# Kernel tuning notes

Hardware: AMD Instinct MI355X
Metric: run time of the kernel (lower is better)

Reference implementation:

```python
import jax, jax.numpy as jnp
import numpy as np

B, T, DM = 4, 1024, 1024
H, NW = 16, 16
HD = DM // H  # 64


def _l2norm(x, eps=1e-12):
    n = jnp.sqrt(jnp.sum(x * x, axis=-1, keepdims=True))
    return x / jnp.maximum(n, eps)


def setup_inputs() -> dict:
    key = jax.random.key(0)
    ks = jax.random.split(key, 14)
    s = 0.02
    d = {
        "x": jax.random.normal(ks[0], (B, T, DM), jnp.float32),
        "Wqf": jax.random.normal(ks[1], (H * NW, DM), jnp.float32) * s,
        "bqf": jnp.zeros((H * NW,), jnp.float32),
        "Wkf": jax.random.normal(ks[2], (H * NW, DM), jnp.float32) * s,
        "bkf": jnp.zeros((H * NW,), jnp.float32),
        "Wqp": jax.random.normal(ks[3], (H * NW, DM), jnp.float32) * s,
        "bqp": jnp.zeros((H * NW,), jnp.float32),
        "Wkp": jax.random.normal(ks[4], (H * NW, DM), jnp.float32) * s,
        "bkp": jnp.zeros((H * NW,), jnp.float32),
        "Wv": jax.random.normal(ks[5], (DM, DM), jnp.float32) * s,
        "bv": jnp.zeros((DM,), jnp.float32),
        "Wo": jax.random.normal(ks[6], (DM, DM), jnp.float32) * s,
        "bo": jnp.zeros((DM,), jnp.float32),
        "inter_scale": jnp.ones((H, 1, 1), jnp.float32),
    }
    return d


def reference(x, Wqf, bqf, Wkf, bkf, Wqp, bqp, Wkp, bkp, Wv, bv, Wo, bo, inter_scale):
    b, t, c = x.shape
    # projections -> [b, H, t, NW]
    def proj(W, bb, w_last):
        return (x @ W.T + bb).reshape(b, t, H, w_last).transpose(0, 2, 1, 3)

    q_f = proj(Wqf, bqf, NW)
    k_f = proj(Wkf, bkf, NW)
    q_p = proj(Wqp, bqp, NW)
    k_p = proj(Wkp, bkp, NW)
    v = proj(Wv, bv, HD)  # [b,H,t,HD]

    t_pos = jnp.arange(t, dtype=x.dtype)[None, None, :, None]  # [1,1,t,1]
    q_waves = jnp.sin(q_f * t_pos + q_p)
    k_waves = jnp.sin(k_f * t_pos + k_p)

    scale_factor = NW ** 0.25
    q_norm = _l2norm(q_waves) * scale_factor
    k_norm = _l2norm(k_waves) * scale_factor

    # wave interference scores [b,H,t,t]
    interference = jnp.einsum('bhtw,bhsw->bhts', q_norm, k_norm)
    interference = interference * inter_scale  # broadcast [H,1,1]

    causal = jnp.tril(jnp.ones((t, t), dtype=bool))  # True = attended
    # elu_plus_one kernel; masked positions -> elu(-inf)+1 == 0
    attn = jnp.where(causal, jax.nn.elu(interference) + 1.0, 0.0)

    num_attended = jnp.arange(1, t + 1, dtype=x.dtype)[None, None, :, None]
    attn = attn / jnp.sqrt(num_attended)

    out = jnp.einsum('bhts,bhsd->bhtd', attn, v)  # [b,H,t,HD]
    out = out.transpose(0, 2, 1, 3).reshape(b, t, c)
    return out @ Wo.T + bo
```

## Files before the change

kernel.cpp:

```cpp
#include <hip/hip_runtime.h>
#include <math.h>

typedef __attribute__((ext_vector_type(8))) short bf16x8;
typedef __attribute__((ext_vector_type(4))) float f32x4;
typedef __attribute__((ext_vector_type(4))) int i32x4;

typedef __attribute__((address_space(3))) void lds_void;
typedef __attribute__((address_space(1))) const void glb_cvoid;

__device__ __forceinline__ unsigned short f32_to_bf16(float f) {
    unsigned u = __float_as_uint(f);
    unsigned r = (u + 0x7FFFu + ((u >> 16) & 1u)) >> 16;
    return (unsigned short)r;
}
__device__ __forceinline__ float bf16_to_f32(unsigned short h) {
    return __uint_as_float(((unsigned)h) << 16);
}

__global__ __launch_bounds__(256)
void split_bf16(const float* __restrict__ src, unsigned short* __restrict__ hi,
                unsigned short* __restrict__ lo, int n4)
{
    const int i = blockIdx.x * 256 + threadIdx.x;
    if (i >= n4) return;
    float4 v = *reinterpret_cast<const float4*>(src + (size_t)i * 4);
    ushort4 h;
    h.x = f32_to_bf16(v.x); h.y = f32_to_bf16(v.y);
    h.z = f32_to_bf16(v.z); h.w = f32_to_bf16(v.w);
    *reinterpret_cast<ushort4*>(hi + (size_t)i * 4) = h;
    if (lo) {
        ushort4 l;
        l.x = f32_to_bf16(v.x - bf16_to_f32(h.x));
        l.y = f32_to_bf16(v.y - bf16_to_f32(h.y));
        l.z = f32_to_bf16(v.z - bf16_to_f32(h.z));
        l.w = f32_to_bf16(v.w - bf16_to_f32(h.w));
        *reinterpret_cast<ushort4*>(lo + (size_t)i * 4) = l;
    }
}

__global__ __launch_bounds__(256)
void split4_bf16(const float* __restrict__ Wqf, const float* __restrict__ Wkf,
                 const float* __restrict__ Wqp, const float* __restrict__ Wkp,
                 unsigned short* __restrict__ WfH, unsigned short* __restrict__ WfL,
                 unsigned short* __restrict__ WpH)
{
    const int i = blockIdx.x * 256 + threadIdx.x;
    const int sel = i >> 16, j = i & 65535;
    const float* W = (sel == 0) ? Wqf : (sel == 1) ? Wkf : (sel == 2) ? Wqp : Wkp;
    float4 v = *reinterpret_cast<const float4*>(W + (size_t)j * 4);
    ushort4 h;
    h.x = f32_to_bf16(v.x); h.y = f32_to_bf16(v.y);
    h.z = f32_to_bf16(v.z); h.w = f32_to_bf16(v.w);
    const size_t o = (size_t)(sel & 1) * 262144 + (size_t)j * 4;
    if (sel < 2) {
        *reinterpret_cast<ushort4*>(WfH + o) = h;
        ushort4 l;
        l.x = f32_to_bf16(v.x - bf16_to_f32(h.x));
        l.y = f32_to_bf16(v.y - bf16_to_f32(h.y));
        l.z = f32_to_bf16(v.z - bf16_to_f32(h.z));
        l.w = f32_to_bf16(v.w - bf16_to_f32(h.w));
        *reinterpret_cast<ushort4*>(WfL + o) = l;
    } else {
        *reinterpret_cast<ushort4*>(WpH + o) = h;
    }
}

__device__ __forceinline__ void xcd_tiles(int& tm, int& tn) {
    const int L = blockIdx.x + gridDim.x * blockIdx.y;
    const int nbn = gridDim.x;
    const int q3 = L >> 3;
    tn = q3 % nbn;
    tm = (L & 7) + 8 * (q3 / nbn);
}

__global__ __launch_bounds__(256)
void freq_gemm_norm(const unsigned short* __restrict__ xh,
                    const unsigned short* __restrict__ xl,
                    const unsigned short* __restrict__ WfH,
                    const unsigned short* __restrict__ WfL,
                    const unsigned short* __restrict__ WpH,
                    const float* __restrict__ bqf, const float* __restrict__ bkf,
                    const float* __restrict__ bqp, const float* __restrict__ bkp,
                    unsigned short* __restrict__ qn, unsigned short* __restrict__ kn)
{
    __shared__ __attribute__((aligned(16))) unsigned short Al[64 * 64];
    __shared__ __attribute__((aligned(16))) unsigned short Bl[64 * 64];

    int tm, tn;
    xcd_tiles(tm, tn);
    const int bm = tm * 64, bn = tn * 64;

    const int tid = threadIdx.x;
    const int w = tid >> 6, l = tid & 63;
    const int wr = w >> 1, wc = w & 1;
    const int lr = l & 15, lg = l >> 4;
    const int r8 = l >> 3;
    const int c8 = l & 7;
    const int csw = (c8 ^ r8) << 3;

    f32x4 accF[2][2], accP[2][2];
#pragma unroll
    for (int i = 0; i < 2; i++)
#pragma unroll
        for (int j = 0; j < 2; j++)
#pragma unroll
            for (int r = 0; r < 4; r++) { accF[i][j][r] = 0.f; accP[i][j][r] = 0.f; }

    for (int k0 = 0; k0 < 4096; k0 += 64) {
        const int seg = k0 >> 10;
        const int kc = k0 & 1023;
        const unsigned short* Aseg = (seg == 1) ? xl : xh;
        const unsigned short* Bseg = (seg <= 1) ? WfH : (seg == 2) ? WfL : WpH;

#pragma unroll
        for (int i = 0; i < 2; i++) {
            __builtin_amdgcn_global_load_lds(
                (glb_cvoid*)(Aseg + (size_t)(bm + w * 16 + i * 8 + r8) * 1024 + kc + csw),
                (lds_void*)(&Al[(w * 16 + i * 8) * 64]), 16, 0, 0);
            __builtin_amdgcn_global_load_lds(
                (glb_cvoid*)(Bseg + (size_t)(bn + w * 16 + i * 8 + r8) * 1024 + kc + csw),
                (lds_void*)(&Bl[(w * 16 + i * 8) * 64]), 16, 0, 0);
        }
        __syncthreads();

        bf16x8 af[2][2], bfr[2][2];
#pragma unroll
        for (int i = 0; i < 2; i++)
#pragma unroll
            for (int kk = 0; kk < 2; kk++) {
                af[i][kk] = *reinterpret_cast<const bf16x8*>(
                    &Al[(wr * 32 + i * 16 + lr) * 64 + (((kk * 4 + lg) ^ (lr & 7)) << 3)]);
                bfr[i][kk] = *reinterpret_cast<const bf16x8*>(
                    &Bl[(wc * 32 + i * 16 + lr) * 64 + (((kk * 4 + lg) ^ (lr & 7)) << 3)]);
            }
        if (seg < 3) {
#pragma unroll
            for (int kk = 0; kk < 2; kk++)
#pragma unroll
                for (int i = 0; i < 2; i++)
#pragma unroll
                    for (int j = 0; j < 2; j++)
                        accF[i][j] = __builtin_amdgcn_mfma_f32_16x16x32_bf16(
                            af[i][kk], bfr[j][kk], accF[i][j], 0, 0, 0);
        } else {
#pragma unroll
            for (int kk = 0; kk < 2; kk++)
#pragma unroll
                for (int i = 0; i < 2; i++)
#pragma unroll
                    for (int j = 0; j < 2; j++)
                        accP[i][j] = __builtin_amdgcn_mfma_f32_16x16x32_bf16(
                            af[i][kk], bfr[j][kk], accP[i][j], 0, 0, 0);
        }
        __syncthreads();
    }

#pragma unroll
    for (int i = 0; i < 2; i++) {
#pragma unroll
        for (int j = 0; j < 2; j++) {
            const int col = bn + wc * 32 + j * 16 + lr;
            const bool isQ = col < 256;
            const int c = col & 255;
            const float bf = isQ ? bqf[c] : bkf[c];
            const float bp = isQ ? bqp[c] : bkp[c];
            unsigned short* dst = isQ ? qn : kn;
            const int h = c >> 4, ww = c & 15;
#pragma unroll
            for (int r = 0; r < 4; r++) {
                const int row = bm + wr * 32 + i * 16 + lg * 4 + r;
                const int b = row >> 10, t = row & 1023;
                const float f = accF[i][j][r] + bf;
                const float p = accP[i][j][r] + bp;
                const float s = sinf(fmaf(f, (float)t, p));
                float n2 = s * s;
#pragma unroll
                for (int off = 8; off >= 1; off >>= 1)
                    n2 += __shfl_xor(n2, off);
                const float val = s * 2.0f / fmaxf(sqrtf(n2), 1e-12f);
                dst[((size_t)(b * 16 + h) * 1024 + t) * 16 + ww] = f32_to_bf16(val);
            }
        }
    }
}

template <int MODE>
__global__ __launch_bounds__(256)
void mfma_gemm(const unsigned short* __restrict__ A0,
               const unsigned short* __restrict__ B0,
               const float* __restrict__ bias,
               float* __restrict__ outF, unsigned short* __restrict__ outH)
{
    __shared__ __attribute__((aligned(16))) unsigned short Al[128 * 64];
    __shared__ __attribute__((aligned(16))) unsigned short Bl[64 * 64];

    int tm, tn;
    xcd_tiles(tm, tn);
    const int bm = tm * 128, bn = tn * 64;

    const int tid = threadIdx.x;
    const int w = tid >> 6, l = tid & 63;
    const int wr = w >> 1, wc = w & 1;
    const int lr = l & 15, lg = l >> 4;
    const int r8 = l >> 3;
    const int c8 = l & 7;
    const int csw = (c8 ^ r8) << 3;

    f32x4 acc[4][2];
#pragma unroll
    for (int i = 0; i < 4; i++)
#pragma unroll
        for (int j = 0; j < 2; j++)
#pragma unroll
            for (int r = 0; r < 4; r++) acc[i][j][r] = 0.f;

    for (int k0 = 0; k0 < 1024; k0 += 64) {
#pragma unroll
        for (int i = 0; i < 4; i++) {
            __builtin_amdgcn_global_load_lds(
                (glb_cvoid*)(A0 + (size_t)(bm + w * 32 + i * 8 + r8) * 1024 + k0 + csw),
                (lds_void*)(&Al[(w * 32 + i * 8) * 64]), 16, 0, 0);
        }
#pragma unroll
        for (int i = 0; i < 2; i++) {
            __builtin_amdgcn_global_load_lds(
                (glb_cvoid*)(B0 + (size_t)(bn + w * 16 + i * 8 + r8) * 1024 + k0 + csw),
                (lds_void*)(&Bl[(w * 16 + i * 8) * 64]), 16, 0, 0);
        }
        __syncthreads();

        bf16x8 af[4][2], bfr[2][2];
#pragma unroll
        for (int i = 0; i < 4; i++)
#pragma unroll
            for (int kk = 0; kk < 2; kk++)
                af[i][kk] = *reinterpret_cast<const bf16x8*>(
                    &Al[(wr * 64 + i * 16 + lr) * 64 + (((kk * 4 + lg) ^ (lr & 7)) << 3)]);
#pragma unroll
        for (int j = 0; j < 2; j++)
#pragma unroll
            for (int kk = 0; kk < 2; kk++)
                bfr[j][kk] = *reinterpret_cast<const bf16x8*>(
                    &Bl[(wc * 32 + j * 16 + lr) * 64 + (((kk * 4 + lg) ^ (lr & 7)) << 3)]);
#pragma unroll
        for (int kk = 0; kk < 2; kk++)
#pragma unroll
            for (int i = 0; i < 4; i++)
#pragma unroll
                for (int j = 0; j < 2; j++)
                    acc[i][j] = __builtin_amdgcn_mfma_f32_16x16x32_bf16(
                        af[i][kk], bfr[j][kk], acc[i][j], 0, 0, 0);
        __syncthreads();
    }

#pragma unroll
    for (int i = 0; i < 4; i++) {
#pragma unroll
        for (int j = 0; j < 2; j++) {
#pragma unroll
            for (int r = 0; r < 4; r++) {
                const int row = bm + wr * 64 + i * 16 + lg * 4 + r;
                const int col = bn + wc * 32 + j * 16 + lr;
                float v = acc[i][j][r] + bias[col];
                if (MODE == 1) {
                    const int hh = col >> 6, d = col & 63;
                    const int b = row >> 10, t = row & 1023;
                    outH[(((size_t)(b * 16 + hh) * 64 + d) * 1024) + t] =
                        f32_to_bf16(v);
                } else {
                    outF[(size_t)row * 1024 + col] = v;
                }
            }
        }
    }
}

__global__ __launch_bounds__(512)
void wave_attn_mfma(const unsigned short* __restrict__ qn,
                    const unsigned short* __restrict__ kn,
                    const unsigned short* __restrict__ vtt,
                    const float* __restrict__ iscale,
                    unsigned short* __restrict__ y)
{
    const int p = blockIdx.x, bh = blockIdx.y;
    const int h = bh & 15, b = bh >> 4;
    const int tid = threadIdx.x;
    const int wq = tid >> 6;
    const int l = tid & 63;
    const int lt = l & 15;
    const int gl = l >> 4;
    const int it = (wq < 4) ? p : (15 - p);
    const int t0w = it * 64 + (wq & 3) * 16;
    const float scale = iscale[h];
    const int tmine = t0w + lt;

    const bf16x8 zero8 = {0, 0, 0, 0, 0, 0, 0, 0};
    const f32x4 zf = {0.f, 0.f, 0.f, 0.f};
    const size_t kb = (size_t)bh * 1024;

    bf16x8 bq = zero8;
    if (gl < 2)
        bq = *reinterpret_cast<const bf16x8*>(&qn[(kb + t0w + lt) * 16 + gl * 8]);

    f32x4 o[4];
#pragma unroll
    for (int jd = 0; jd < 4; jd++) o[jd] = zf;

    const int addr0 = ((2 * (gl & 1)) * 16 + lt) * 4;
    const int addr1 = addr0 + 64;
    const bool hi = ((gl >> 1) & 1) != 0;

    bf16x8 akc[4], akn[4];
#pragma unroll
    for (int js = 0; js < 4; js++) {
        akc[js] = zero8;
        if (gl < 2)
            akc[js] = *reinterpret_cast<const bf16x8*>(
                &kn[(kb + js * 16 + lt) * 16 + gl * 8]);
    }

    for (int is = 0; is <= it; is++) {
        const int s0 = is * 64;

        if (is < it) {
#pragma unroll
            for (int js = 0; js < 4; js++) {
                akn[js] = zero8;
                if (gl < 2)
                    akn[js] = *reinterpret_cast<const bf16x8*>(
                        &kn[(kb + s0 + 64 + js * 16 + lt) * 16 + gl * 8]);
            }
        }
        bf16x8 bv[2][4];
#pragma unroll
        for (int ks = 0; ks < 2; ks++)
#pragma unroll
            for (int jd = 0; jd < 4; jd++)
                bv[ks][jd] = *reinterpret_cast<const bf16x8*>(
                    &vtt[((size_t)(bh * 64 + jd * 16 + lt)) * 1024 +
                         s0 + ks * 32 + gl * 8]);

        f32x4 st[4];
#pragma unroll
        for (int js = 0; js < 4; js++)
            st[js] = __builtin_amdgcn_mfma_f32_16x16x32_bf16(
                akc[js], bq, zf, 0, 0, 0);

        int pk[4][2];
#pragma unroll
        for (int js = 0; js < 4; js++) {
            float pp[4];
#pragma unroll
            for (int r = 0; r < 4; r++) {
                const int s = s0 + js * 16 + gl * 4 + r;
                const float xv = st[js][r] * scale;
                const float phi = (xv > 0.f) ? (xv + 1.0f) : __expf(xv);
                pp[r] = (s <= tmine) ? phi : 0.f;
            }
            asm("v_cvt_pk_bf16_f32 %0, %1, %2"
                : "=v"(pk[js][0]) : "v"(pp[0]), "v"(pp[1]));
            asm("v_cvt_pk_bf16_f32 %0, %1, %2"
                : "=v"(pk[js][1]) : "v"(pp[2]), "v"(pp[3]));
        }

        int rg[4][2][2];
#pragma unroll
        for (int js = 0; js < 4; js++)
#pragma unroll
            for (int sl = 0; sl < 2; sl++) {
                rg[js][sl][0] = __builtin_amdgcn_ds_bpermute(addr0, pk[js][sl]);
                rg[js][sl][1] = __builtin_amdgcn_ds_bpermute(addr1, pk[js][sl]);
            }

#pragma unroll
        for (int ks = 0; ks < 2; ks++) {
            i32x4 au;
#pragma unroll
            for (int c = 0; c < 2; c++)
#pragma unroll
                for (int sl = 0; sl < 2; sl++)
                    au[2 * c + sl] = hi ? rg[2 * ks + 1][sl][c]
                                        : rg[2 * ks][sl][c];
            const bf16x8 pa = __builtin_bit_cast(bf16x8, au);
#pragma unroll
            for (int jd = 0; jd < 4; jd++)
                o[jd] = __builtin_amdgcn_mfma_f32_16x16x32_bf16(
                    pa, bv[ks][jd], o[jd], 0, 0, 0);
        }

#pragma unroll
        for (int js = 0; js < 4; js++) akc[js] = akn[js];
    }

#pragma unroll
    for (int r = 0; r < 4; r++) {
        const int t = t0w + gl * 4 + r;
        const float inv = rsqrtf((float)(t + 1));
#pragma unroll
        for (int jd = 0; jd < 4; jd++) {
            const int d = jd * 16 + lt;
            y[((size_t)b * 1024 + t) * 1024 + h * 64 + d] =
                f32_to_bf16(o[jd][r] * inv);
        }
    }
}

extern "C" void kernel_launch(void* const* d_in, const int* in_sizes, int n_in,
                              void* d_out, int out_size, void* d_ws, size_t ws_size,
                              hipStream_t stream)
{
    const float* x   = (const float*)d_in[0];
    const float* Wqf = (const float*)d_in[1];
    const float* bqf = (const float*)d_in[2];
    const float* Wkf = (const float*)d_in[3];
    const float* bkf = (const float*)d_in[4];
    const float* Wqp = (const float*)d_in[5];
    const float* bqp = (const float*)d_in[6];
    const float* Wkp = (const float*)d_in[7];
    const float* bkp = (const float*)d_in[8];
    const float* Wv  = (const float*)d_in[9];
    const float* bv  = (const float*)d_in[10];
    const float* Wo  = (const float*)d_in[11];
    const float* bo  = (const float*)d_in[12];
    const float* isc = (const float*)d_in[13];
    float* out = (float*)d_out;

    char* ws = (char*)d_ws;
    unsigned short* ybf = (unsigned short*)(ws);
    unsigned short* qn  = (unsigned short*)(ws + ( 8u << 20));
    unsigned short* kn  = (unsigned short*)(ws + (10u << 20));
    unsigned short* WfH = (unsigned short*)(ws + (12u << 20));
    unsigned short* WfL = (unsigned short*)(ws + (13u << 20));
    unsigned short* WpH = (unsigned short*)(ws + (14u << 20));
    unsigned short* xh  = (unsigned short*)(ws + (16u << 20));
    unsigned short* xl  = (unsigned short*)(ws + (24u << 20));
    unsigned short* vtt = (unsigned short*)(ws + (24u << 20));
    unsigned short* WvH = (unsigned short*)(ws + (32u << 20));
    unsigned short* WoH = WvH;

    split_bf16<<<4096, 256, 0, stream>>>(x, xh, xl, 1048576);
    split4_bf16<<<1024, 256, 0, stream>>>(Wqf, Wkf, Wqp, Wkp, WfH, WfL, WpH);

    freq_gemm_norm<<<dim3(8, 64), 256, 0, stream>>>(
        xh, xl, WfH, WfL, WpH, bqf, bkf, bqp, bkp, qn, kn);

    split_bf16<<<1024, 256, 0, stream>>>(Wv, WvH, nullptr, 262144);
    mfma_gemm<1><<<dim3(16, 32), 256, 0, stream>>>(xh, WvH, bv, nullptr, vtt);

    wave_attn_mfma<<<dim3(8, 64), 512, 0, stream>>>(qn, kn, vtt, isc, ybf);

    split_bf16<<<1024, 256, 0, stream>>>(Wo, WoH, nullptr, 262144);
    mfma_gemm<2><<<dim3(16, 32), 256, 0, stream>>>(ybf, WoH, bo, out, nullptr);
}
```

Measured before the change: 227.2 us.

## Double-buffer LDS tiles in projection GEMMs and use fast sine intrinsic

Both the frequency/phase GEMM and the generic MFMA GEMM now use two LDS buffers. The next K-tile is prefetched with global_load_lds while the current tile feeds the MFMAs, using explicit vmcnt waits and raw barriers in place of __syncthreads, so global load latency overlaps compute. The epilogue switches sinf to __sinf. Arguments reach magnitudes near 1000, so the hardware sine's range reduction may lose accuracy. An unused fast_sin helper is also added.

```diff
diff --git a/kernel.cpp b/kernel.cpp
--- a/kernel.cpp
+++ b/kernel.cpp
@@ -73,6 +73,11 @@
     tm = (L & 7) + 8 * (q3 / nbn);
 }
 
+__device__ __forceinline__ float fast_sin(float x) {
+    float r = x * 0.15915494309189535f;
+    return __sinf(r * 6.2831853071795865f) * 0.f + __sinf(x);
+}
+
 __global__ __launch_bounds__(256)
 void freq_gemm_norm(const unsigned short* __restrict__ xh,
                     const unsigned short* __restrict__ xl,
@@ -83,8 +88,8 @@
                     const float* __restrict__ bqp, const float* __restrict__ bkp,
                     unsigned short* __restrict__ qn, unsigned short* __restrict__ kn)
 {
-    __shared__ __attribute__((aligned(16))) unsigned short Al[64 * 64];
-    __shared__ __attribute__((aligned(16))) unsigned short Bl[64 * 64];
+    __shared__ __attribute__((aligned(16))) unsigned short Al[2 * 64 * 64];
+    __shared__ __attribute__((aligned(16))) unsigned short Bl[2 * 64 * 64];
 
     int tm, tn;
     xcd_tiles(tm, tn);
@@ -106,34 +111,49 @@
 #pragma unroll
             for (int r = 0; r < 4; r++) { accF[i][j][r] = 0.f; accP[i][j][r] = 0.f; }
 
-    for (int k0 = 0; k0 < 4096; k0 += 64) {
-        const int seg = k0 >> 10;
-        const int kc = k0 & 1023;
+    auto stage = [&](int t, int buf) {
+        const int seg = t >> 4;
+        const int kc = (t << 6) & 1023;
         const unsigned short* Aseg = (seg == 1) ? xl : xh;
         const unsigned short* Bseg = (seg <= 1) ? WfH : (seg == 2) ? WfL : WpH;
-
+        unsigned short* Ad = Al + buf * 4096;
+        unsigned short* Bd = Bl + buf * 4096;
 #pragma unroll
         for (int i = 0; i < 2; i++) {
             __builtin_amdgcn_global_load_lds(
                 (glb_cvoid*)(Aseg + (size_t)(bm + w * 16 + i * 8 + r8) * 1024 + kc + csw),
-                (lds_void*)(&Al[(w * 16 + i * 8) * 64]), 16, 0, 0);
+                (lds_void*)(&Ad[(w * 16 + i * 8) * 64]), 16, 0, 0);
             __builtin_amdgcn_global_load_lds(
                 (glb_cvoid*)(Bseg + (size_t)(bn + w * 16 + i * 8 + r8) * 1024 + kc + csw),
-                (lds_void*)(&Bl[(w * 16 + i * 8) * 64]), 16, 0, 0);
-        }
-        __syncthreads();
-
+                (lds_void*)(&Bd[(w * 16 + i * 8) * 64]), 16, 0, 0);
+        }
+    };
+
+    stage(0, 0);
+    for (int t = 0; t < 64; ++t) {
+        const int cur = t & 1;
+        if (t < 63) {
+            stage(t + 1, cur ^ 1);
+            asm volatile("s_waitcnt vmcnt(4)" ::: "memory");
+        } else {
+            asm volatile("s_waitcnt vmcnt(0)" ::: "memory");
+        }
+        __builtin_amdgcn_s_barrier();
+        asm volatile("" ::: "memory");
+
+        const unsigned short* Ac = Al + cur * 4096;
+        const unsigned short* Bc = Bl + cur * 4096;
         bf16x8 af[2][2], bfr[2][2];
 #pragma unroll
         for (int i = 0; i < 2; i++)
 #pragma unroll
             for (int kk = 0; kk < 2; kk++) {
                 af[i][kk] = *reinterpret_cast<const bf16x8*>(
-                    &Al[(wr * 32 + i * 16 + lr) * 64 + (((kk * 4 + lg) ^ (lr & 7)) << 3)]);
+                    &Ac[(wr * 32 + i * 16 + lr) * 64 + (((kk * 4 + lg) ^ (lr & 7)) << 3)]);
                 bfr[i][kk] = *reinterpret_cast<const bf16x8*>(
-                    &Bl[(wc * 32 + i * 16 + lr) * 64 + (((kk * 4 + lg) ^ (lr & 7)) << 3)]);
-            }
-        if (seg < 3) {
+                    &Bc[(wc * 32 + i * 16 + lr) * 64 + (((kk * 4 + lg) ^ (lr & 7)) << 3)]);
+            }
+        if ((t >> 4) < 3) {
 #pragma unroll
             for (int kk = 0; kk < 2; kk++)
 #pragma unroll
@@ -152,7 +172,8 @@
                         accP[i][j] = __builtin_amdgcn_mfma_f32_16x16x32_bf16(
                             af[i][kk], bfr[j][kk], accP[i][j], 0, 0, 0);
         }
-        __syncthreads();
+        __builtin_amdgcn_s_barrier();
+        asm volatile("" ::: "memory");
     }
 
 #pragma unroll
@@ -172,7 +193,7 @@
                 const int b = row >> 10, t = row & 1023;
                 const float f = accF[i][j][r] + bf;
                 const float p = accP[i][j][r] + bp;
-                const float s = sinf(fmaf(f, (float)t, p));
+                const float s = __sinf(fmaf(f, (float)t, p));
                 float n2 = s * s;
 #pragma unroll
                 for (int off = 8; off >= 1; off >>= 1)
@@ -191,8 +212,8 @@
                const float* __restrict__ bias,
                float* __restrict__ outF, unsigned short* __restrict__ outH)
 {
-    __shared__ __attribute__((aligned(16))) unsigned short Al[128 * 64];
-    __shared__ __attribute__((aligned(16))) unsigned short Bl[64 * 64];
+    __shared__ __attribute__((aligned(16))) unsigned short Al[2 * 128 * 64];
+    __shared__ __attribute__((aligned(16))) unsigned short Bl[2 * 64 * 64];
 
     int tm, tn;
     xcd_tiles(tm, tn);
@@ -214,34 +235,49 @@
 #pragma unroll
             for (int r = 0; r < 4; r++) acc[i][j][r] = 0.f;
 
-    for (int k0 = 0; k0 < 1024; k0 += 64) {
-#pragma unroll
-        for (int i = 0; i < 4; i++) {
+    auto stage = [&](int t, int buf) {
+        const int k0 = t << 6;
+        unsigned short* Ad = Al + buf * 8192;
+        unsigned short* Bd = Bl + buf * 4096;
+#pragma unroll
+        for (int i = 0; i < 4; i++)
             __builtin_amdgcn_global_load_lds(
                 (glb_cvoid*)(A0 + (size_t)(bm + w * 32 + i * 8 + r8) * 1024 + k0 + csw),
-                (lds_void*)(&Al[(w * 32 + i * 8) * 64]), 16, 0, 0);
-        }
-#pragma unroll
-        for (int i = 0; i < 2; i++) {
+                (lds_void*)(&Ad[(w * 32 + i * 8) * 64]), 16, 0, 0);
+#pragma unroll
+        for (int i = 0; i < 2; i++)
             __builtin_amdgcn_global_load_lds(
                 (glb_cvoid*)(B0 + (size_t)(bn + w * 16 + i * 8 + r8) * 1024 + k0 + csw),
-                (lds_void*)(&Bl[(w * 16 + i * 8) * 64]), 16, 0, 0);
-        }
-        __syncthreads();
-
+                (lds_void*)(&Bd[(w * 16 + i * 8) * 64]), 16, 0, 0);
+    };
+
+    stage(0, 0);
+    for (int t = 0; t < 16; ++t) {
+        const int cur = t & 1;
+        if (t < 15) {
+            stage(t + 1, cur ^ 1);
+            asm volatile("s_waitcnt vmcnt(6)" ::: "memory");
+        } else {
+            asm volatile("s_waitcnt vmcnt(0)" ::: "memory");
+        }
+        __builtin_amdgcn_s_barrier();
+        asm volatile("" ::: "memory");
+
+        const unsigned short* Ac = Al + cur * 8192;
+        const unsigned short* Bc = Bl + cur * 4096;
         bf16x8 af[4][2], bfr[2][2];
 #pragma unroll
         for (int i = 0; i < 4; i++)
 #pragma unroll
             for (int kk = 0; kk < 2; kk++)
                 af[i][kk] = *reinterpret_cast<const bf16x8*>(
-                    &Al[(wr * 64 + i * 16 + lr) * 64 + (((kk * 4 + lg) ^ (lr & 7)) << 3)]);
+                    &Ac[(wr * 64 + i * 16 + lr) * 64 + (((kk * 4 + lg) ^ (lr & 7)) << 3)]);
 #pragma unroll
         for (int j = 0; j < 2; j++)
 #pragma unroll
             for (int kk = 0; kk < 2; kk++)
                 bfr[j][kk] = *reinterpret_cast<const bf16x8*>(
-                    &Bl[(wc * 32 + j * 16 + lr) * 64 + (((kk * 4 + lg) ^ (lr & 7)) << 3)]);
+                    &Bc[(wc * 32 + j * 16 + lr) * 64 + (((kk * 4 + lg) ^ (lr & 7)) << 3)]);
 #pragma unroll
         for (int kk = 0; kk < 2; kk++)
 #pragma unroll
@@ -250,7 +286,8 @@
                 for (int j = 0; j < 2; j++)
                     acc[i][j] = __builtin_amdgcn_mfma_f32_16x16x32_bf16(
                         af[i][kk], bfr[j][kk], acc[i][j], 0, 0, 0);
-        __syncthreads();
+        __builtin_amdgcn_s_barrier();
+        asm volatile("" ::: "memory");
     }
 
 #pragma unroll
```

Measured after the change: 250.1 us. +10.1%, slower.
